# Optimization experiments

Measured on AMD Instinct MI355X. Metric: run time of the kernel, lower is better.

The kernel has to match this reference:

```python
import jax, jax.numpy as jnp
import numpy as np

T = 32        # time_step
H = 64        # n_hidden (and dense width)
A = 8         # nb_actions
OBS_DIM = 512
B = 4096      # sequences; obs rows = B*T
LN_EPS = 1e-12  # tf.contrib.layers.layer_norm epsilon


def setup_inputs() -> dict:
    key = jax.random.key(0)
    ks = jax.random.split(key, 10)
    s = 0.1
    return {
        "obs":  jax.random.normal(ks[0], (B * T, OBS_DIM), jnp.float32),
        "W0":   jax.random.normal(ks[1], (OBS_DIM, H), jnp.float32) * s,
        "b0":   jnp.zeros((H,), jnp.float32),
        "gamma": jnp.ones((H,), jnp.float32),
        "beta":  jnp.zeros((H,), jnp.float32),
        "Wfw":  jax.random.normal(ks[2], (2 * H, 4 * H), jnp.float32) * s,
        "bfw":  jnp.zeros((4 * H,), jnp.float32),
        "Wbw":  jax.random.normal(ks[3], (2 * H, 4 * H), jnp.float32) * s,
        "bbw":  jnp.zeros((4 * H,), jnp.float32),
        "Wc":   jax.random.uniform(ks[4], (H, A), jnp.float32, -0.003, 0.003),
        "bc":   jnp.zeros((A,), jnp.float32),
    }


def _lstm_scan(xs, W, b):
    """BasicLSTMCell (forget_bias=1.0). xs: [T, B, H] -> hs: [T, B, H]."""
    nb = xs.shape[1]
    init = (jnp.zeros((nb, H), xs.dtype), jnp.zeros((nb, H), xs.dtype))

    def step(carry, x_t):
        c, h = carry
        z = jnp.concatenate([x_t, h], axis=-1) @ W + b  # [B, 4H]
        i, j, f, o = jnp.split(z, 4, axis=-1)           # TF gate order i,j,f,o
        c = c * jax.nn.sigmoid(f + 1.0) + jax.nn.sigmoid(i) * jnp.tanh(j)
        h = jnp.tanh(c) * jax.nn.sigmoid(o)
        return (c, h), h

    _, hs = jax.lax.scan(step, init, xs)
    return hs


def reference(obs, W0, b0, gamma, beta, Wfw, bfw, Wbw, bbw, Wc, bc):
    # dense(64) + layer_norm + relu
    x = obs @ W0 + b0                                   # [B*T, H]
    mu = jnp.mean(x, axis=-1, keepdims=True)
    var = jnp.mean(jnp.square(x - mu), axis=-1, keepdims=True)
    x = gamma * (x - mu) / jnp.sqrt(var + LN_EPS) + beta
    x = jax.nn.relu(x)

    xt = x.reshape(-1, T, H).transpose(1, 0, 2)          # [T, B, H]
    hs_fw = _lstm_scan(xt, Wfw, bfw)                     # [T, B, H]
    hs_bw = _lstm_scan(xt[::-1], Wbw, bbw)[::-1]         # reverse-in, reverse-out

    # tf.reshape on the (fw, bw) tuple stacks along a new leading axis:
    # [2, B, T, H] -> [2B, T*H, 1]; conv1d(kernel=stride=H) == per-step proj.
    y = jnp.stack([hs_fw.transpose(1, 0, 2), hs_bw.transpose(1, 0, 2)], axis=0)
    y = y.reshape(-1, T, H)                              # [2B, T, H]
    out = jnp.tanh(jnp.einsum('btk,ka->bta', y, Wc) + bc)  # [2B, T, A]
    return out
```

## Files before the change

### kernel.cpp

```cpp
#include <hip/hip_runtime.h>
#include <hip/hip_bf16.h>

typedef __attribute__((ext_vector_type(8))) short bf16x8;
typedef __attribute__((ext_vector_type(4))) float f32x4;

#define MFMA_BF16 __builtin_amdgcn_mfma_f32_16x16x32_bf16

#define GLDS16(gp, lp)                                                        \
  __builtin_amdgcn_global_load_lds(                                           \
      (const __attribute__((address_space(1))) void*)(gp),                    \
      (__attribute__((address_space(3))) void*)(lp), 16, 0, 0)

__device__ __forceinline__ unsigned pk2(float a, float b) {
  __hip_bfloat162 t = __float22bfloat162_rn(make_float2(a, b));
  return *reinterpret_cast<unsigned*>(&t);
}
__device__ __forceinline__ unsigned short f2bf_hw(float f) {
  __hip_bfloat16 h = __float2bfloat16(f);
  return *reinterpret_cast<unsigned short*>(&h);
}
__device__ __forceinline__ float sigm(float x) {
  return __builtin_amdgcn_rcpf(1.f + __expf(-x));
}
__device__ __forceinline__ float tanh_f(float x) {
  return 1.f - 2.f * __builtin_amdgcn_rcpf(1.f + __expf(2.f * x));
}

__global__ void k0_conv(const float* __restrict__ W0, const float* __restrict__ Wfw,
                        const float* __restrict__ Wbw, unsigned short* __restrict__ wfrag,
                        unsigned short* __restrict__ wlstm) {
  int gid = blockIdx.x * 256 + threadIdx.x;
  if (gid < 4096) {
    int f = gid >> 6, l = gid & 63;
    int k0 = (f >> 2) * 32 + ((l >> 4) << 3);
    int n = (f & 3) * 16 + (l & 15);
    bf16x8 v;
#pragma unroll
    for (int j = 0; j < 8; ++j) v[j] = (short)f2bf_hw(W0[(k0 + j) * 64 + n]);
    *(bf16x8*)(wfrag + gid * 8) = v;
  } else if (gid < 12288) {
    int g2 = gid - 4096;
    const float* W = (g2 < 4096) ? Wfw : Wbw;
    int f = (g2 & 4095) >> 6, l = g2 & 63;
    int wv = f >> 4, gate = (f >> 2) & 3, kf = f & 3;
    int col = gate * 64 + wv * 16 + (l & 15);
    int kr = kf * 32 + ((l >> 4) << 3);
    bf16x8 v;
#pragma unroll
    for (int j = 0; j < 8; ++j) v[j] = (short)f2bf_hw(W[(kr + j) * 256 + col]);
    *(bf16x8*)(wlstm + g2 * 8) = v;
  }
}

__global__ __launch_bounds__(256, 2) void k_dense_ln(
    const float* __restrict__ obs, const unsigned short* __restrict__ wfrag,
    const float* __restrict__ b0, const float* __restrict__ gam,
    const float* __restrict__ bet, unsigned short* __restrict__ xout) {
  __shared__ __align__(16) char lds[65536];
  const int tid = threadIdx.x, w = tid >> 6, l = tid & 63;
  const int g = l >> 4, c = l & 15;
  const long blk64 = (long)blockIdx.x * 64;
  const long rb = blk64 + w * 16;

  float b0v[4], gv[4], bv[4];
#pragma unroll
  for (int nt = 0; nt < 4; ++nt) {
    int col = nt * 16 + c;
    b0v[nt] = b0[col]; gv[nt] = gam[col]; bv[nt] = bet[col];
  }
  const unsigned short* wfl = wfrag + l * 8;

  const int sr0 = w * 16 + (l >> 5);
  const int su = l & 31;
  const char* gB = (const char*)obs + blk64 * 2048;

  asm volatile("s_waitcnt vmcnt(0)" ::: "memory");

#define K1_STAGE(q)                                                           \
  {                                                                           \
    _Pragma("unroll") for (int i = 0; i < 8; ++i) {                           \
      int r_ = sr0 + 2 * i;                                                   \
      int chk_ = su ^ (r_ & 7);                                               \
      const char* gp_ = gB + (long)r_ * 2048 + (q) * 512 + chk_ * 16;         \
      char* lp_ = lds + ((q) & 1) * 32768 + (w * 512 + i * 64) * 16;          \
      GLDS16(gp_, lp_);                                                       \
    }                                                                         \
  }

  K1_STAGE(0);
  K1_STAGE(1);

  f32x4 acc[4];
#pragma unroll
  for (int nt = 0; nt < 4; ++nt) acc[nt] = (f32x4){0.f, 0.f, 0.f, 0.f};

#pragma unroll
  for (int q = 0; q < 4; ++q) {
    if (q < 3) asm volatile("s_waitcnt vmcnt(8)" ::: "memory");
    else       asm volatile("s_waitcnt vmcnt(0)" ::: "memory");
    __builtin_amdgcn_s_barrier();
    __builtin_amdgcn_sched_barrier(0);

    const char* bufb = lds + (q & 1) * 32768 + (w * 16 + c) * 512;
#pragma unroll
    for (int kf2 = 0; kf2 < 4; ++kf2) {
      bf16x8 B0 = *(const bf16x8*)(wfl + ((q * 4 + kf2) * 4 + 0) * 512);
      bf16x8 B1 = *(const bf16x8*)(wfl + ((q * 4 + kf2) * 4 + 1) * 512);
      bf16x8 B2 = *(const bf16x8*)(wfl + ((q * 4 + kf2) * 4 + 2) * 512);
      bf16x8 B3 = *(const bf16x8*)(wfl + ((q * 4 + kf2) * 4 + 3) * 512);
      int v0 = kf2 * 8 + g * 2;
      float4 f0 = *(const float4*)(bufb + ((v0 + 0) ^ (c & 7)) * 16);
      float4 f1 = *(const float4*)(bufb + ((v0 + 1) ^ (c & 7)) * 16);
      union { bf16x8 v; unsigned u[4]; } af;
      af.u[0] = pk2(f0.x, f0.y); af.u[1] = pk2(f0.z, f0.w);
      af.u[2] = pk2(f1.x, f1.y); af.u[3] = pk2(f1.z, f1.w);
      acc[0] = MFMA_BF16(af.v, B0, acc[0], 0, 0, 0);
      acc[1] = MFMA_BF16(af.v, B1, acc[1], 0, 0, 0);
      acc[2] = MFMA_BF16(af.v, B2, acc[2], 0, 0, 0);
      acc[3] = MFMA_BF16(af.v, B3, acc[3], 0, 0, 0);
    }
    if (q < 2) {
      __builtin_amdgcn_s_barrier();
      __builtin_amdgcn_sched_barrier(0);
      K1_STAGE(q + 2);
    }
  }

  float vv[4][4], s1[4], s2[4];
#pragma unroll
  for (int r = 0; r < 4; ++r) { s1[r] = 0.f; s2[r] = 0.f; }
#pragma unroll
  for (int nt = 0; nt < 4; ++nt)
#pragma unroll
    for (int r = 0; r < 4; ++r) {
      float val = acc[nt][r] + b0v[nt];
      vv[nt][r] = val; s1[r] += val; s2[r] += val * val;
    }
#pragma unroll
  for (int r = 0; r < 4; ++r) {
#pragma unroll
    for (int m = 1; m <= 8; m <<= 1) {
      s1[r] += __shfl_xor(s1[r], m);
      s2[r] += __shfl_xor(s2[r], m);
    }
  }
  unsigned short* xw = (unsigned short*)lds + w * 1024;
#pragma unroll
  for (int r = 0; r < 4; ++r) {
    float mu = s1[r] * 0.015625f;
    float var = s2[r] * 0.015625f - mu * mu;
    float inv = rsqrtf(var + 1e-12f);
    int row = g * 4 + r;
#pragma unroll
    for (int nt = 0; nt < 4; ++nt) {
      float xn = (vv[nt][r] - mu) * inv * gv[nt] + bv[nt];
      xw[(row * 64 + nt * 16 + c) ^ (g << 3)] = f2bf_hw(fmaxf(xn, 0.f));
    }
  }
#pragma unroll
  for (int m2 = 0; m2 < 2; ++m2) {
    int m = m2 * 64 + l;
    int row = m >> 3, u8 = m & 7;
    bf16x8 v = *(const bf16x8*)(xw + ((row * 64 + u8 * 8) ^ ((row >> 2) << 3)));
    *(bf16x8*)(xout + (rb + row) * 64 + u8 * 8) = v;
  }
}

__global__ __launch_bounds__(256, 2) void k_lstm(
    const unsigned short* __restrict__ x, const unsigned short* __restrict__ wlstm,
    const float* __restrict__ bfw, const float* __restrict__ bbw,
    const float* __restrict__ Wc, const float* __restrict__ bc,
    float* __restrict__ out) {
  __shared__ __align__(16) char xl[65536];
  __shared__ unsigned short hl[2 * 1024];
  const int tid = threadIdx.x, w = tid >> 6, l = tid & 63;
  const int g = l >> 4, c = l & 15;
  const int dir = blockIdx.x >> 8;
  const int sq = (blockIdx.x & 255) * 16;
  const float* bias = dir ? bbw : bfw;

  bf16x8 Bf[4][4];
  const unsigned short* wl = wlstm + ((long)dir * 4096 + w * 16 * 64) * 8;
#pragma unroll
  for (int gate = 0; gate < 4; ++gate)
#pragma unroll
    for (int kf = 0; kf < 4; ++kf)
      Bf[gate][kf] = *(const bf16x8*)(wl + ((gate * 4 + kf) * 64 + l) * 8);
  float bz[4];
#pragma unroll
  for (int gate = 0; gate < 4; ++gate) bz[gate] = bias[gate * 64 + w * 16 + c];

  bf16x8 Pc[2];
#pragma unroll
  for (int kf = 0; kf < 2; ++kf)
#pragma unroll
    for (int j = 0; j < 8; ++j) Pc[kf][j] = 0;
  float bcv = 0.f;
  if (w == 0 && c < 8) {
#pragma unroll
    for (int kf = 0; kf < 2; ++kf)
#pragma unroll
      for (int j = 0; j < 8; ++j)
        Pc[kf][j] = (short)f2bf_hw(Wc[(kf * 32 + g * 8 + j) * 8 + c]);
    bcv = bc[c];
  }

  asm volatile("s_waitcnt vmcnt(0)" ::: "memory");

  const int ss = l >> 3, sc = l & 7;
#pragma unroll
  for (int j = 0; j < 8; ++j) {
    int tt = w * 8 + j;
    int te = dir ? 31 - tt : tt;
#pragma unroll
    for (int p = 0; p < 2; ++p) {
      int s = p * 8 + ss;
      const char* gp = (const char*)x +
          ((long)(sq + s) * 32 + te) * 128 + (long)(sc ^ (s & 7)) * 16;
      char* lp = xl + tt * 2048 + p * 1024;
      GLDS16(gp, lp);
    }
  }

  for (int i = tid; i < 1024; i += 256) ((unsigned*)hl)[i] = 0u;
  float cs[4] = {0.f, 0.f, 0.f, 0.f};

  if (w == 0) asm volatile("s_waitcnt vmcnt(14)" ::: "memory");
  asm volatile("s_waitcnt lgkmcnt(0)" ::: "memory");
  __builtin_amdgcn_s_barrier();
  __builtin_amdgcn_sched_barrier(0);

  const int hq = w >> 1;
  const int hgp = ((w & 1) * 2 + (c >> 3)) * 16;
  const int hlo = c & 7;

  int p = 0;
#pragma unroll
  for (int t = 0; t < 32; ++t) {
    const int te = dir ? 31 - t : t;
    const char* xt = xl + t * 2048 + c * 128;
    bf16x8 Ax0 = *(const bf16x8*)(xt + (long)((g) ^ (c & 7)) * 16);
    bf16x8 Ax1 = *(const bf16x8*)(xt + (long)((4 + g) ^ (c & 7)) * 16);
    bf16x8 Ah0 = *(const bf16x8*)((const char*)hl + p * 2048 + l * 16);
    bf16x8 Ah1 = *(const bf16x8*)((const char*)hl + p * 2048 + 1024 + l * 16);

    f32x4 acc[4];
#pragma unroll
    for (int gate = 0; gate < 4; ++gate)
      acc[gate] = (f32x4){bz[gate], bz[gate], bz[gate], bz[gate]};
#pragma unroll
    for (int gate = 0; gate < 4; ++gate) {
      acc[gate] = MFMA_BF16(Ax0, Bf[gate][0], acc[gate], 0, 0, 0);
      acc[gate] = MFMA_BF16(Ax1, Bf[gate][1], acc[gate], 0, 0, 0);
      acc[gate] = MFMA_BF16(Ah0, Bf[gate][2], acc[gate], 0, 0, 0);
      acc[gate] = MFMA_BF16(Ah1, Bf[gate][3], acc[gate], 0, 0, 0);
    }

    const int wb = (p ^ 1) * 1024;
#pragma unroll
    for (int r = 0; r < 4; ++r) {
      float si = sigm(acc[0][r]);
      float tj = tanh_f(acc[1][r]);
      float sf = sigm(acc[2][r] + 1.f);
      float so = sigm(acc[3][r]);
      cs[r] = cs[r] * sf + si * tj;
      hl[wb + (hq * 64 + hgp + 4 * g + r) * 8 + hlo] = f2bf_hw(tanh_f(cs[r]) * so);
    }

    if (t + 1 < 32) {
      if (w == ((t + 1) >> 3))
        asm volatile("s_waitcnt vmcnt(%0)" :: "i"(14 - 2 * ((t + 1) & 7)) : "memory");
    }
    asm volatile("s_waitcnt lgkmcnt(0)" ::: "memory");
    __builtin_amdgcn_s_barrier();
    __builtin_amdgcn_sched_barrier(0);

    if (w == 0 && t >= 1) {
      f32x4 pa = (f32x4){0.f, 0.f, 0.f, 0.f};
      pa = MFMA_BF16(Ah0, Pc[0], pa, 0, 0, 0);
      pa = MFMA_BF16(Ah1, Pc[1], pa, 0, 0, 0);
      if (c < 8) {
        int tp = dir ? 32 - t : t - 1;
#pragma unroll
        for (int r = 0; r < 4; ++r) {
          long orow = (long)dir * 4096 + sq + 4 * g + r;
          out[(orow * 32 + tp) * 8 + c] = tanh_f(pa[r] + bcv);
        }
      }
    }
    p ^= 1;
  }

  if (w == 0) {
    bf16x8 Ph0 = *(const bf16x8*)((const char*)hl + p * 2048 + l * 16);
    bf16x8 Ph1 = *(const bf16x8*)((const char*)hl + p * 2048 + 1024 + l * 16);
    f32x4 pa = (f32x4){0.f, 0.f, 0.f, 0.f};
    pa = MFMA_BF16(Ph0, Pc[0], pa, 0, 0, 0);
    pa = MFMA_BF16(Ph1, Pc[1], pa, 0, 0, 0);
    if (c < 8) {
      int tp = dir ? 0 : 31;
#pragma unroll
      for (int r = 0; r < 4; ++r) {
        long orow = (long)dir * 4096 + sq + 4 * g + r;
        out[(orow * 32 + tp) * 8 + c] = tanh_f(pa[r] + bcv);
      }
    }
  }
}

extern "C" void kernel_launch(void* const* d_in, const int* in_sizes, int n_in,
                              void* d_out, int out_size, void* d_ws, size_t ws_size,
                              hipStream_t stream) {
  const float* obs = (const float*)d_in[0];
  const float* W0  = (const float*)d_in[1];
  const float* b0  = (const float*)d_in[2];
  const float* gam = (const float*)d_in[3];
  const float* bet = (const float*)d_in[4];
  const float* Wfw = (const float*)d_in[5];
  const float* bfw = (const float*)d_in[6];
  const float* Wbw = (const float*)d_in[7];
  const float* bbw = (const float*)d_in[8];
  const float* Wc  = (const float*)d_in[9];
  const float* bc  = (const float*)d_in[10];
  float* out = (float*)d_out;

  unsigned short* wfrag = (unsigned short*)d_ws;
  unsigned short* wlstm = wfrag + 4096 * 8;
  unsigned short* xbf   = wlstm + 8192 * 8;

  k0_conv<<<48, 256, 0, stream>>>(W0, Wfw, Wbw, wfrag, wlstm);
  k_dense_ln<<<2048, 256, 0, stream>>>(obs, wfrag, b0, gam, bet, xbf);
  k_lstm<<<512, 256, 0, stream>>>(xbf, wlstm, bfw, bbw, Wc, bc, out);
}
```

Measured before the change: 103.9 us.

## Triple-buffer dense stage and precompute next-step input gates in LSTM

The dense+LayerNorm kernel now streams the K dimension in eight smaller chunks through three LDS buffers. That shrinks LDS to 48KB and raises the occupancy target to 3 blocks per SM, with deeper prefetch. In the LSTM recurrence, the input-projection MFMAs for step t+1 are issued off the critical path while step t's gates are computed, and the wait on x loads shifts one step ahead. Gate nonlinearities are fused to share reciprocals, which cuts rcp count but may change numerics slightly; the output tanh switches to library tanhf.

```diff
diff --git a/kernel.cpp b/kernel.cpp
--- a/kernel.cpp
+++ b/kernel.cpp
@@ -18,12 +18,6 @@
 __device__ __forceinline__ unsigned short f2bf_hw(float f) {
   __hip_bfloat16 h = __float2bfloat16(f);
   return *reinterpret_cast<unsigned short*>(&h);
-}
-__device__ __forceinline__ float sigm(float x) {
-  return __builtin_amdgcn_rcpf(1.f + __expf(-x));
-}
-__device__ __forceinline__ float tanh_f(float x) {
-  return 1.f - 2.f * __builtin_amdgcn_rcpf(1.f + __expf(2.f * x));
 }
 
 __global__ void k0_conv(const float* __restrict__ W0, const float* __restrict__ Wfw,
@@ -52,11 +46,11 @@
   }
 }
 
-__global__ __launch_bounds__(256, 2) void k_dense_ln(
+__global__ __launch_bounds__(256, 3) void k_dense_ln(
     const float* __restrict__ obs, const unsigned short* __restrict__ wfrag,
     const float* __restrict__ b0, const float* __restrict__ gam,
     const float* __restrict__ bet, unsigned short* __restrict__ xout) {
-  __shared__ __align__(16) char lds[65536];
+  __shared__ __align__(16) char lds[49152];
   const int tid = threadIdx.x, w = tid >> 6, l = tid & 63;
   const int g = l >> 4, c = l & 15;
   const long blk64 = (long)blockIdx.x * 64;
@@ -69,48 +63,48 @@
     b0v[nt] = b0[col]; gv[nt] = gam[col]; bv[nt] = bet[col];
   }
   const unsigned short* wfl = wfrag + l * 8;
-
-  const int sr0 = w * 16 + (l >> 5);
-  const int su = l & 31;
   const char* gB = (const char*)obs + blk64 * 2048;
 
+  const int rlo = w * 4 + g;
   asm volatile("s_waitcnt vmcnt(0)" ::: "memory");
 
 #define K1_STAGE(q)                                                           \
   {                                                                           \
-    _Pragma("unroll") for (int i = 0; i < 8; ++i) {                           \
-      int r_ = sr0 + 2 * i;                                                   \
-      int chk_ = su ^ (r_ & 7);                                               \
-      const char* gp_ = gB + (long)r_ * 2048 + (q) * 512 + chk_ * 16;         \
-      char* lp_ = lds + ((q) & 1) * 32768 + (w * 512 + i * 64) * 16;          \
+    _Pragma("unroll") for (int i = 0; i < 4; ++i) {                           \
+      int row_ = i * 16 + rlo;                                                \
+      const char* gp_ = gB + (long)row_ * 2048 + (q) * 256 +                  \
+                        (long)((c ^ rlo) * 16);                               \
+      char* lp_ = lds + ((q) % 3) * 16384 + (i * 4096 + (w * 64 + l) * 16);   \
       GLDS16(gp_, lp_);                                                       \
     }                                                                         \
   }
 
   K1_STAGE(0);
   K1_STAGE(1);
+  K1_STAGE(2);
 
   f32x4 acc[4];
 #pragma unroll
   for (int nt = 0; nt < 4; ++nt) acc[nt] = (f32x4){0.f, 0.f, 0.f, 0.f};
 
 #pragma unroll
-  for (int q = 0; q < 4; ++q) {
-    if (q < 3) asm volatile("s_waitcnt vmcnt(8)" ::: "memory");
-    else       asm volatile("s_waitcnt vmcnt(0)" ::: "memory");
+  for (int q = 0; q < 8; ++q) {
+    constexpr int VW[8] = {8, 16, 24, 24, 24, 24, 20, 16};
+    asm volatile("s_waitcnt vmcnt(%0)" :: "i"(VW[q]) : "memory");
     __builtin_amdgcn_s_barrier();
     __builtin_amdgcn_sched_barrier(0);
 
-    const char* bufb = lds + (q & 1) * 32768 + (w * 16 + c) * 512;
-#pragma unroll
-    for (int kf2 = 0; kf2 < 4; ++kf2) {
-      bf16x8 B0 = *(const bf16x8*)(wfl + ((q * 4 + kf2) * 4 + 0) * 512);
-      bf16x8 B1 = *(const bf16x8*)(wfl + ((q * 4 + kf2) * 4 + 1) * 512);
-      bf16x8 B2 = *(const bf16x8*)(wfl + ((q * 4 + kf2) * 4 + 2) * 512);
-      bf16x8 B3 = *(const bf16x8*)(wfl + ((q * 4 + kf2) * 4 + 3) * 512);
-      int v0 = kf2 * 8 + g * 2;
-      float4 f0 = *(const float4*)(bufb + ((v0 + 0) ^ (c & 7)) * 16);
-      float4 f1 = *(const float4*)(bufb + ((v0 + 1) ^ (c & 7)) * 16);
+    const char* rowb = lds + (q % 3) * 16384 + (w * 16 + c) * 256;
+#pragma unroll
+    for (int kf = 0; kf < 2; ++kf) {
+      int fb = (q * 2 + kf) * 4;
+      bf16x8 B0 = *(const bf16x8*)(wfl + (fb + 0) * 512);
+      bf16x8 B1 = *(const bf16x8*)(wfl + (fb + 1) * 512);
+      bf16x8 B2 = *(const bf16x8*)(wfl + (fb + 2) * 512);
+      bf16x8 B3 = *(const bf16x8*)(wfl + (fb + 3) * 512);
+      int u0 = kf * 8 + g * 2;
+      float4 f0 = *(const float4*)(rowb + ((u0 + 0) ^ c) * 16);
+      float4 f1 = *(const float4*)(rowb + ((u0 + 1) ^ c) * 16);
       union { bf16x8 v; unsigned u[4]; } af;
       af.u[0] = pk2(f0.x, f0.y); af.u[1] = pk2(f0.z, f0.w);
       af.u[2] = pk2(f1.x, f1.y); af.u[3] = pk2(f1.z, f1.w);
@@ -119,10 +113,10 @@
       acc[2] = MFMA_BF16(af.v, B2, acc[2], 0, 0, 0);
       acc[3] = MFMA_BF16(af.v, B3, acc[3], 0, 0, 0);
     }
-    if (q < 2) {
+    if (q < 5) {
       __builtin_amdgcn_s_barrier();
       __builtin_amdgcn_sched_barrier(0);
-      K1_STAGE(q + 2);
+      K1_STAGE(q + 3);
     }
   }
 
@@ -225,7 +219,7 @@
   for (int i = tid; i < 1024; i += 256) ((unsigned*)hl)[i] = 0u;
   float cs[4] = {0.f, 0.f, 0.f, 0.f};
 
-  if (w == 0) asm volatile("s_waitcnt vmcnt(14)" ::: "memory");
+  if (w == 0) asm volatile("s_waitcnt vmcnt(12)" ::: "memory");
   asm volatile("s_waitcnt lgkmcnt(0)" ::: "memory");
   __builtin_amdgcn_s_barrier();
   __builtin_amdgcn_sched_barrier(0);
@@ -234,48 +228,72 @@
   const int hgp = ((w & 1) * 2 + (c >> 3)) * 16;
   const int hlo = c & 7;
 
-  int p = 0;
-#pragma unroll
-  for (int t = 0; t < 32; ++t) {
-    const int te = dir ? 31 - t : t;
-    const char* xt = xl + t * 2048 + c * 128;
+  f32x4 accx[4];
+  {
+    const char* xt = xl + 0 * 2048 + c * 128;
     bf16x8 Ax0 = *(const bf16x8*)(xt + (long)((g) ^ (c & 7)) * 16);
     bf16x8 Ax1 = *(const bf16x8*)(xt + (long)((4 + g) ^ (c & 7)) * 16);
+#pragma unroll
+    for (int gate = 0; gate < 4; ++gate) {
+      f32x4 b = (f32x4){bz[gate], bz[gate], bz[gate], bz[gate]};
+      accx[gate] = MFMA_BF16(Ax1, Bf[gate][1],
+                             MFMA_BF16(Ax0, Bf[gate][0], b, 0, 0, 0), 0, 0, 0);
+    }
+  }
+
+  int p = 0;
+#pragma unroll
+  for (int t = 0; t < 32; ++t) {
     bf16x8 Ah0 = *(const bf16x8*)((const char*)hl + p * 2048 + l * 16);
     bf16x8 Ah1 = *(const bf16x8*)((const char*)hl + p * 2048 + 1024 + l * 16);
 
     f32x4 acc[4];
 #pragma unroll
     for (int gate = 0; gate < 4; ++gate)
-      acc[gate] = (f32x4){bz[gate], bz[gate], bz[gate], bz[gate]};
-#pragma unroll
-    for (int gate = 0; gate < 4; ++gate) {
-      acc[gate] = MFMA_BF16(Ax0, Bf[gate][0], acc[gate], 0, 0, 0);
-      acc[gate] = MFMA_BF16(Ax1, Bf[gate][1], acc[gate], 0, 0, 0);
-      acc[gate] = MFMA_BF16(Ah0, Bf[gate][2], acc[gate], 0, 0, 0);
-      acc[gate] = MFMA_BF16(Ah1, Bf[gate][3], acc[gate], 0, 0, 0);
+      acc[gate] = MFMA_BF16(Ah1, Bf[gate][3],
+                            MFMA_BF16(Ah0, Bf[gate][2], accx[gate], 0, 0, 0),
+                            0, 0, 0);
+
+    if (t + 1 < 32) {
+      const char* xt = xl + (t + 1) * 2048 + c * 128;
+      bf16x8 Ax0 = *(const bf16x8*)(xt + (long)((g) ^ (c & 7)) * 16);
+      bf16x8 Ax1 = *(const bf16x8*)(xt + (long)((4 + g) ^ (c & 7)) * 16);
+#pragma unroll
+      for (int gate = 0; gate < 4; ++gate) {
+        f32x4 b = (f32x4){bz[gate], bz[gate], bz[gate], bz[gate]};
+        accx[gate] = MFMA_BF16(Ax1, Bf[gate][1],
+                               MFMA_BF16(Ax0, Bf[gate][0], b, 0, 0, 0), 0, 0, 0);
+      }
     }
 
     const int wb = (p ^ 1) * 1024;
 #pragma unroll
     for (int r = 0; r < 4; ++r) {
-      float si = sigm(acc[0][r]);
-      float tj = tanh_f(acc[1][r]);
-      float sf = sigm(acc[2][r] + 1.f);
-      float so = sigm(acc[3][r]);
-      cs[r] = cs[r] * sf + si * tj;
-      hl[wb + (hq * 64 + hgp + 4 * g + r) * 8 + hlo] = f2bf_hw(tanh_f(cs[r]) * so);
-    }
-
-    if (t + 1 < 32) {
-      if (w == ((t + 1) >> 3))
-        asm volatile("s_waitcnt vmcnt(%0)" :: "i"(14 - 2 * ((t + 1) & 7)) : "memory");
+      float ei = __expf(-acc[0][r]);
+      float ej = __expf(2.f * acc[1][r]);
+      float ef = __expf(-(acc[2][r] + 1.f));
+      float eo = __expf(-acc[3][r]);
+      float p12 = (1.f + ei) * (1.f + ej);
+      float r3 = __builtin_amdgcn_rcpf(p12 * (1.f + ef));
+      float it = (ej - 1.f) * (1.f + ef) * r3;
+      float sf = p12 * r3;
+      cs[r] = cs[r] * sf + it;
+      float ec = __expf(2.f * cs[r]);
+      float r2 = __builtin_amdgcn_rcpf((1.f + eo) * (1.f + ec));
+      hl[wb + (hq * 64 + hgp + 4 * g + r) * 8 + hlo] =
+          f2bf_hw((ec - 1.f) * r2);
+    }
+
+    if (t + 2 < 32) {
+      if (w == ((t + 2) >> 3))
+        asm volatile("s_waitcnt vmcnt(%0)" :: "i"(14 - 2 * ((t + 2) & 7)) : "memory");
     }
     asm volatile("s_waitcnt lgkmcnt(0)" ::: "memory");
     __builtin_amdgcn_s_barrier();
     __builtin_amdgcn_sched_barrier(0);
 
     if (w == 0 && t >= 1) {
+      int te = dir ? 31 - t : t;
       f32x4 pa = (f32x4){0.f, 0.f, 0.f, 0.f};
       pa = MFMA_BF16(Ah0, Pc[0], pa, 0, 0, 0);
       pa = MFMA_BF16(Ah1, Pc[1], pa, 0, 0, 0);
@@ -284,7 +302,7 @@
 #pragma unroll
         for (int r = 0; r < 4; ++r) {
           long orow = (long)dir * 4096 + sq + 4 * g + r;
-          out[(orow * 32 + tp) * 8 + c] = tanh_f(pa[r] + bcv);
+          out[(orow * 32 + tp) * 8 + c] = tanhf(pa[r] + bcv);
         }
       }
     }
@@ -302,7 +320,7 @@
 #pragma unroll
       for (int r = 0; r < 4; ++r) {
         long orow = (long)dir * 4096 + sq + 4 * g + r;
-        out[(orow * 32 + tp) * 8 + c] = tanh_f(pa[r] + bcv);
+        out[(orow * 32 + tp) * 8 + c] = tanhf(pa[r] + bcv);
       }
     }
   }
```

New measurement: 102.3 us. About the same (-1.6%).
